# Performance work log

Hardware: AMD Instinct MI355X
Metric: run time of the kernel (lower is better)

The kernel has to match this reference:

```python
import jax, jax.numpy as jnp
import numpy as np

T, H = 2048, 2048            # tokens, hidden_size
NQ, NKV, D = 32, 4, 128      # q heads, kv heads, head_dim
E, K, I, CAP = 64, 8, 768, 512  # experts, top_k, moe_intermediate, per-expert capacity
EPS, THETA = 1e-6, 10000.0


def setup_inputs() -> dict:
    key = jax.random.key(0)
    ks = jax.random.split(key, 10)
    n = lambda k, shp, sc: jax.random.normal(k, shp, jnp.float32) * sc
    return {
        "hidden_states": n(ks[0], (T, H), 1.0),
        "positions": jnp.arange(T, dtype=jnp.int32),
        "wqkv": n(ks[1], (H, (NQ + 2 * NKV) * D), H ** -0.5),
        "wo": n(ks[2], (NQ * D, H), (NQ * D) ** -0.5),
        "q_norm_w": jnp.ones((D,), jnp.float32),
        "k_norm_w": jnp.ones((D,), jnp.float32),
        "ln1_w": jnp.ones((H,), jnp.float32),
        "ln2_w": jnp.ones((H,), jnp.float32),
        "gate_w": n(ks[3], (H, E), H ** -0.5),
        "w_gate": n(ks[4], (E, H, I), H ** -0.5),
        "w_up": n(ks[5], (E, H, I), H ** -0.5),
        "w_down": n(ks[6], (E, I, H), I ** -0.5),
    }


def _rmsnorm(x, w):
    v = jnp.mean(jnp.square(x.astype(jnp.float32)), axis=-1, keepdims=True)
    return (x.astype(jnp.float32) * jax.lax.rsqrt(v + EPS)).astype(x.dtype) * w


def _rope(x, cos, sin):
    # x: [T, heads, D]; neox-style rotate-half over full head_dim
    x1, x2 = x[..., : D // 2], x[..., D // 2:]
    c, s = cos[:, None, :], sin[:, None, :]
    return jnp.concatenate([x1 * c - x2 * s, x2 * c + x1 * s], axis=-1)


def _forward(hidden_states, positions, wqkv, wo, q_norm_w, k_norm_w, ln1_w, ln2_w, gate_w, w_gate, w_up, w_down):
    x = hidden_states
    # ---- input RMSNorm + GQA attention with QK-norm + RoPE ----
    h = _rmsnorm(x, ln1_w)
    qkv = h @ wqkv
    q, k, v = jnp.split(qkv, [NQ * D, NQ * D + NKV * D], axis=-1)
    q = _rmsnorm(q.reshape(T, NQ, D), q_norm_w)
    k = _rmsnorm(k.reshape(T, NKV, D), k_norm_w)
    v = v.reshape(T, NKV, D)
    inv_freq = 1.0 / (THETA ** (jnp.arange(0, D, 2, dtype=jnp.float32) / D))
    ang = positions.astype(jnp.float32)[:, None] * inv_freq  # [T, D/2]
    cos, sin = jnp.cos(ang), jnp.sin(ang)
    q, k = _rope(q, cos, sin), _rope(k, cos, sin)
    rep = NQ // NKV
    kr = jnp.repeat(k, rep, axis=1)  # [T, NQ, D]
    vr = jnp.repeat(v, rep, axis=1)
    scores = jnp.einsum('qhd,khd->hqk', q, kr) * (D ** -0.5)
    causal = jnp.tril(jnp.ones((T, T), bool))
    scores = jnp.where(causal[None], scores, -1e30)
    probs = jax.nn.softmax(scores, axis=-1)
    attn = jnp.einsum('hqk,khd->qhd', probs, vr).reshape(T, NQ * D)
    x = x + attn @ wo
    # ---- post-attn RMSNorm + sparse MoE (softmax top-k routing, renormalized) ----
    h = _rmsnorm(x, ln2_w)
    logits = h @ gate_w
    gate_probs = jax.nn.softmax(logits.astype(jnp.float32), axis=-1)
    topk_w, topk_idx = jax.lax.top_k(gate_probs, K)              # [T, K]
    topk_w = topk_w / jnp.sum(topk_w, axis=-1, keepdims=True)    # norm_topk_prob
    flat_e = topk_idx.reshape(-1)                                # [T*K], row-major
    oh = jax.nn.one_hot(flat_e, E, dtype=jnp.int32)
    pos = jnp.sum(jnp.cumsum(oh, axis=0) * oh, axis=-1) - 1      # slot within expert
    x_rep = jnp.repeat(h, K, axis=0)                             # [T*K, H]
    buf = jnp.zeros((E, CAP, H), h.dtype).at[flat_e, pos].set(x_rep, mode='drop')
    g = jnp.einsum('ech,ehi->eci', buf, w_gate)
    u = jnp.einsum('ech,ehi->eci', buf, w_up)
    act = jax.nn.silu(g) * u
    out_buf = jnp.einsum('eci,eih->ech', act, w_down)
    valid = (pos < CAP).astype(h.dtype)                          # CAP >> expected load; no drops in practice
    gathered = out_buf[flat_e, jnp.clip(pos, 0, CAP - 1)]        # [T*K, H]
    w = topk_w.reshape(-1).astype(h.dtype) * valid
    moe_out = jnp.sum((gathered * w[:, None]).reshape(T, K, H), axis=1)
    return x + moe_out


def reference(hidden_states, positions, wqkv, wo, q_norm_w, k_norm_w, ln1_w, ln2_w, gate_w, w_gate, w_up, w_down):
    return _forward(hidden_states, positions, wqkv, wo, q_norm_w, k_norm_w,
                    ln1_w, ln2_w, gate_w, w_gate, w_up, w_down)
```

## Files before the change

### kernel.cpp

```cpp
#include <hip/hip_runtime.h>
#include <hip/hip_bf16.h>

#define T_    2048
#define H_    2048
#define NQ_   32
#define NKV_  4
#define D_    128
#define E_    64
#define TK_   8
#define I_    768
#define CAP_  512
#define QKVW_ 5120

typedef float  f32x4  __attribute__((ext_vector_type(4)));
typedef __bf16 bf16x8 __attribute__((ext_vector_type(8)));
typedef int    i32x4  __attribute__((ext_vector_type(4)));
#define AS1 __attribute__((address_space(1)))
#define AS3 __attribute__((address_space(3)))

static __device__ __forceinline__ unsigned f2bf_u(float f){
  unsigned u = __builtin_bit_cast(unsigned, f);
  u += 0x7fffu + ((u >> 16) & 1u);
  return u >> 16;
}
static __device__ __forceinline__ float bf2f(unsigned h){
  unsigned u = h << 16;
  return __builtin_bit_cast(float, u);
}
struct HL { int h; int l; };
static __device__ __forceinline__ HL packsplit(float a, float b){
  unsigned ah = f2bf_u(a), bh = f2bf_u(b);
  float al = a - bf2f(ah), bl = b - bf2f(bh);
  HL r;
  r.h = (int)(ah | (bh << 16));
  r.l = (int)(f2bf_u(al) | (f2bf_u(bl) << 16));
  return r;
}
static __device__ __forceinline__ f32x4 mfma16(bf16x8 a, bf16x8 b, f32x4 c){
  return __builtin_amdgcn_mfma_f32_16x16x32_bf16(a, b, c, 0, 0, 0);
}

__global__ __launch_bounds__(256) void k_rms(const float* __restrict__ in,
                                             const float* __restrict__ w,
                                             unsigned short* __restrict__ outh,
                                             unsigned short* __restrict__ outl,
                                             float* __restrict__ cpy)
{
  const int t = blockIdx.x, tid = threadIdx.x;
  const float* row = in + (long)t * H_;
  float4 a = *(const float4*)(row + tid*8);
  float4 b = *(const float4*)(row + tid*8 + 4);
  float ss = a.x*a.x + a.y*a.y + a.z*a.z + a.w*a.w
           + b.x*b.x + b.y*b.y + b.z*b.z + b.w*b.w;
  #pragma unroll
  for (int o = 32; o >= 1; o >>= 1) ss += __shfl_xor(ss, o);
  __shared__ float red[4];
  if ((tid & 63) == 0) red[tid >> 6] = ss;
  __syncthreads();
  float tot = red[0] + red[1] + red[2] + red[3];
  float rs = rsqrtf(tot * (1.0f / (float)H_) + 1e-6f);
  const float* wp = w + tid*8;
  float vv[8] = {a.x, a.y, a.z, a.w, b.x, b.y, b.z, b.w};
  i32x4 oh, ol;
  #pragma unroll
  for (int d = 0; d < 4; d++){
    float v0 = vv[2*d]   * rs * wp[2*d];
    float v1 = vv[2*d+1] * rs * wp[2*d+1];
    HL r = packsplit(v0, v1);
    oh[d] = r.h; ol[d] = r.l;
  }
  *(i32x4*)(outh + (long)t * H_ + tid*8) = oh;
  if (outl) *(i32x4*)(outl + (long)t * H_ + tid*8) = ol;
  if (cpy){
    *(float4*)(cpy + (long)t * H_ + tid*8)     = a;
    *(float4*)(cpy + (long)t * H_ + tid*8 + 4) = b;
  }
}

__global__ __launch_bounds__(64) void k_ropetab(const int* __restrict__ pos,
                                                float* __restrict__ cosb,
                                                float* __restrict__ sinb)
{
  int t = blockIdx.x, j = threadIdx.x;
  float p = (float)pos[t];
  float freq = expf(-(float)j * (2.0f / (float)D_) * 9.210340371976184f);
  float ang = p * freq;
  cosb[t*64 + j] = cosf(ang);
  sinb[t*64 + j] = sinf(ang);
}

__global__ __launch_bounds__(256) void k_qknorm(const float* __restrict__ qkv,
                                                const float* __restrict__ qw,
                                                const float* __restrict__ kw,
                                                const float* __restrict__ cosb,
                                                const float* __restrict__ sinb,
                                                unsigned short* __restrict__ qh,
                                                unsigned short* __restrict__ ql,
                                                unsigned short* __restrict__ khp,
                                                unsigned short* __restrict__ klp)
{
  int gw = blockIdx.x*4 + (threadIdx.x >> 6);
  int lane = threadIdx.x & 63;
  int t = gw / 36, hh = gw - t*36;
  const float* src; const float* w;
  unsigned short *dh, *dl;
  if (hh < NQ_){
    src = qkv + (long)t*QKVW_ + hh*D_;
    w = qw;
    dh = qh + ((long)t*NQ_ + hh)*D_;
    dl = ql + ((long)t*NQ_ + hh)*D_;
  } else {
    int kh = hh - NQ_;
    src = qkv + (long)t*QKVW_ + NQ_*D_ + kh*D_;
    w = kw;
    dh = khp + ((long)t*NKV_ + kh)*D_;
    dl = klp + ((long)t*NKV_ + kh)*D_;
  }
  float a = src[lane], b = src[lane + 64];
  float ss = a*a + b*b;
  #pragma unroll
  for (int o = 32; o >= 1; o >>= 1) ss += __shfl_xor(ss, o);
  float rs = rsqrtf(ss * (1.0f / (float)D_) + 1e-6f);
  a *= rs * w[lane];
  b *= rs * w[lane + 64];
  float c = cosb[t*64 + lane], s = sinb[t*64 + lane];
  float r0 = a*c - b*s;
  float r1 = b*c + a*s;
  unsigned h0 = f2bf_u(r0), h1 = f2bf_u(r1);
  dh[lane]      = (unsigned short)h0;
  dh[lane + 64] = (unsigned short)h1;
  dl[lane]      = (unsigned short)f2bf_u(r0 - bf2f(h0));
  dl[lane + 64] = (unsigned short)f2bf_u(r1 - bf2f(h1));
}

__global__ __launch_bounds__(256) void k_vtrans(const float* __restrict__ qkv,
                                                unsigned short* __restrict__ vth,
                                                unsigned short* __restrict__ vtl)
{
  __shared__ unsigned short tileh[64][136];
  __shared__ unsigned short tilel[64][136];
  const int t0 = blockIdx.x * 64;
  const int hv = blockIdx.y;
  const int tid = threadIdx.x;
  #pragma unroll
  for (int it = 0; it < 8; it++){
    int chunk = tid + it*256;
    int r  = chunk >> 5;
    int c4 = chunk & 31;
    float4 v = *(const float4*)(qkv + (long)(t0 + r)*QKVW_ + (NQ_+NKV_)*D_ + hv*D_ + c4*4);
    float vals[4] = {v.x, v.y, v.z, v.w};
    #pragma unroll
    for (int q = 0; q < 4; q++){
      unsigned hi = f2bf_u(vals[q]);
      tileh[r][c4*4+q] = (unsigned short)hi;
      tilel[r][c4*4+q] = (unsigned short)f2bf_u(vals[q] - bf2f(hi));
    }
  }
  __syncthreads();
  int d = tid >> 1, hf = tid & 1;
  long dbase = ((long)(hv*D_ + d))*T_ + t0 + hf*32;
  #pragma unroll
  for (int k = 0; k < 4; k++){
    i32x4 oh, ol;
    #pragma unroll
    for (int d2 = 0; d2 < 4; d2++){
      int r0 = hf*32 + k*8 + d2*2, r1 = r0 + 1;
      oh[d2] = (int)((unsigned)tileh[r0][d] | ((unsigned)tileh[r1][d] << 16));
      ol[d2] = (int)((unsigned)tilel[r0][d] | ((unsigned)tilel[r1][d] << 16));
    }
    *(i32x4*)(vth + dbase + k*8) = oh;
    *(i32x4*)(vtl + dbase + k*8) = ol;
  }
}

__global__ __launch_bounds__(256,2) void k_attn(const unsigned short* __restrict__ qbh,
                                                const unsigned short* __restrict__ qbl,
                                                const unsigned short* __restrict__ kbh,
                                                const unsigned short* __restrict__ kbl,
                                                const unsigned short* __restrict__ vth,
                                                const unsigned short* __restrict__ vtl,
                                                unsigned short* __restrict__ abh,
                                                unsigned short* __restrict__ abl)
{
  __shared__ char ldsK[2][2][16384];
  const int b   = blockIdx.x;
  const int xcd = b & 7, kk = xcd >> 1;
  const int s_  = ((b >> 3) << 1) | (xcd & 1);
  const int h   = kk*8 + (s_ >> 4);
  const int p   = s_ & 15;
  const int hk  = kk;
  const int tid = threadIdx.x;
  const int wv  = tid >> 6, lane = tid & 63;
  const int l15 = lane & 15, g16 = lane >> 4;
  const float sc = 0.08838834764831845f;

  long gb[4];
  #pragma unroll
  for (int i = 0; i < 4; i++){
    int srow = i*16 + (tid >> 4);
    int c = (tid & 15) ^ (srow & 7);
    gb[i] = ((long)srow*NKV_ + hk)*D_ + c*8;
  }

  for (int ph = 0; ph < 2; ph++){
    const int qt  = ph ? p : (31 - p);
    const int q0  = qt*64 + wv*16;
    const int ntB = qt + 1;

    bf16x8 qfh[4], qfl[4];
    {
      long qoff = ((long)(q0 + l15)*NQ_ + h)*D_ + g16*8;
      #pragma unroll
      for (int ks = 0; ks < 4; ks++){
        qfh[ks] = *(const bf16x8*)(qbh + qoff + ks*32);
        qfl[ks] = *(const bf16x8*)(qbl + qoff + ks*32);
      }
    }

    f32x4 zz = {0.f,0.f,0.f,0.f};
    f32x4 o[8];
    #pragma unroll
    for (int dn = 0; dn < 8; dn++) o[dn] = zz;
    float m_run = -1e30f, l_run = 0.f;

    __syncthreads();
    #pragma unroll
    for (int i = 0; i < 4; i++){
      __builtin_amdgcn_global_load_lds((const AS1 int*)(kbh + gb[i]),
          (AS3 int*)((AS3 char*)&ldsK[0][0][0] + i*4096 + tid*16), 16, 0, 0);
      __builtin_amdgcn_global_load_lds((const AS1 int*)(kbl + gb[i]),
          (AS3 int*)((AS3 char*)&ldsK[0][1][0] + i*4096 + tid*16), 16, 0, 0);
    }

    for (int t = 0; t < ntB; t++){
      __syncthreads();
      const int kv0 = t*64;
      if (t+1 < ntB){
        long kadd = (long)(t+1)*64*NKV_*D_;
        int nb = (t+1) & 1;
        #pragma unroll
        for (int i = 0; i < 4; i++){
          __builtin_amdgcn_global_load_lds((const AS1 int*)(kbh + gb[i] + kadd),
              (AS3 int*)((AS3 char*)&ldsK[nb][0][0] + i*4096 + tid*16), 16, 0, 0);
          __builtin_amdgcn_global_load_lds((const AS1 int*)(kbl + gb[i] + kadd),
              (AS3 int*)((AS3 char*)&ldsK[nb][1][0] + i*4096 + tid*16), 16, 0, 0);
        }
      }
      {
        const char* Kh = &ldsK[t & 1][0][0];
        const char* Kl = &ldsK[t & 1][1][0];
        f32x4 sA[4];
        #pragma unroll
        for (int sub = 0; sub < 4; sub++) sA[sub] = zz;
        __builtin_amdgcn_s_setprio(1);
        #pragma unroll
        for (int sub = 0; sub < 4; sub++){
          int row = sub*16 + l15;
          int rsw = (row & 7) << 4;
          #pragma unroll
          for (int ks = 0; ks < 4; ks++){
            bf16x8 kh = *(const bf16x8*)(Kh + row*256 + (((ks*4 + g16)*16) ^ rsw));
            bf16x8 kl = *(const bf16x8*)(Kl + row*256 + (((ks*4 + g16)*16) ^ rsw));
            sA[sub] = mfma16(kh, qfl[ks], sA[sub]);
            sA[sub] = mfma16(kl, qfh[ks], sA[sub]);
            sA[sub] = mfma16(kh, qfh[ks], sA[sub]);
          }
        }
        __builtin_amdgcn_s_setprio(0);
        {
          int qrow = q0 + l15;
          float mt = -1e30f;
          #pragma unroll
          for (int sub = 0; sub < 4; sub++)
            #pragma unroll
            for (int r = 0; r < 4; r++){
              int kva = kv0 + sub*16 + g16*4 + r;
              float v = sA[sub][r]*sc;
              if (kva > qrow) v = -1e30f;
              sA[sub][r] = v;
              mt = fmaxf(mt, v);
            }
          mt = fmaxf(mt, __shfl_xor(mt,16));
          mt = fmaxf(mt, __shfl_xor(mt,32));
          float mnew = fmaxf(m_run, mt);
          float corr = __expf(m_run - mnew);
          float ps = 0.f;
          #pragma unroll
          for (int sub = 0; sub < 4; sub++)
            #pragma unroll
            for (int r = 0; r < 4; r++){
              float e = __expf(sA[sub][r] - mnew);
              sA[sub][r] = e;
              ps += e;
            }
          ps += __shfl_xor(ps,16);
          ps += __shfl_xor(ps,32);
          l_run = l_run*corr + ps;
          m_run = mnew;
          #pragma unroll
          for (int r = 0; r < 4; r++){
            float cr = __shfl(corr, g16*4 + r);
            #pragma unroll
            for (int dn = 0; dn < 8; dn++) o[dn][r] *= cr;
          }
        }
        #pragma unroll
        for (int kst = 0; kst < 2; kst++){
          bf16x8 pah, pal;
          {
            f32x4 s0 = sA[2*kst], s1 = sA[2*kst+1];
            i32x4 pkh, pkl;
            #pragma unroll
            for (int d = 0; d < 4; d++){
              const int e0 = 2*d, e1 = 2*d+1;
              int src0 = (((2*g16 + (e0>>2)) & 3) << 4) | l15;
              int src1 = (((2*g16 + (e1>>2)) & 3) << 4) | l15;
              float a0t = __shfl(s0[e0&3], src0), a1t = __shfl(s1[e0&3], src0);
              float b0t = __shfl(s0[e1&3], src1), b1t = __shfl(s1[e1&3], src1);
              float va = (g16 >= 2) ? a1t : a0t;
              float vb = (g16 >= 2) ? b1t : b0t;
              HL r = packsplit(va, vb);
              pkh[d] = r.h; pkl[d] = r.l;
            }
            pah = __builtin_bit_cast(bf16x8, pkh);
            pal = __builtin_bit_cast(bf16x8, pkl);
          }
          __builtin_amdgcn_s_setprio(1);
          #pragma unroll
          for (int dn = 0; dn < 8; dn++){
            long voff = ((long)(hk*D_ + dn*16 + l15))*T_ + kv0 + kst*32 + g16*8;
            bf16x8 bvh = *(const bf16x8*)(vth + voff);
            bf16x8 bvl = *(const bf16x8*)(vtl + voff);
            o[dn] = mfma16(pah, bvl, o[dn]);
            o[dn] = mfma16(pal, bvh, o[dn]);
            o[dn] = mfma16(pah, bvh, o[dn]);
          }
          __builtin_amdgcn_s_setprio(0);
        }
      }
    }

    {
      float linv = 1.0f / l_run;
      #pragma unroll
      for (int r = 0; r < 4; r++){
        float lr = __shfl(linv, g16*4 + r);
        long row = q0 + g16*4 + r;
        #pragma unroll
        for (int dn = 0; dn < 8; dn++){
          float v = o[dn][r]*lr;
          unsigned hi = f2bf_u(v);
          long idx = row*(NQ_*D_) + h*D_ + dn*16 + l15;
          abh[idx] = (unsigned short)hi;
          abl[idx] = (unsigned short)f2bf_u(v - bf2f(hi));
        }
      }
    }
  }
}

struct SA {
  const unsigned short* Ah;
  const unsigned short* Al;
  const float* B;
  int lda, ldb, K, ldc;
  float* Cf;
  const float* add;
};

template<int MODE>
__global__ __launch_bounds__(256,2) void k_gs(SA ga)
{
  __shared__ unsigned short ldsAh[128*64];
  __shared__ unsigned short ldsAl[128*64];
  __shared__ unsigned short ldsBh[8*128*8];
  __shared__ unsigned short ldsBl[8*128*8];
  const int tid = threadIdx.x;
  const int lane = tid & 63;
  const int wv = tid >> 6;
  const int wm = (wv >> 1)*64, wn = (wv & 1)*64;
  const int l15 = lane & 15, g16 = lane >> 4;

  const long m0 = (long)blockIdx.y * 128;
  const long n0 = (long)blockIdx.x * 128;

  long aoff[4];
  #pragma unroll
  for (int i = 0; i < 4; i++){
    int chunk = tid + i*256;
    int m = chunk >> 3, c = chunk & 7;
    aoff[i] = (m0 + m) * (long)ga.lda + c*8;
  }
  const float* brow = ga.B + n0 + (long)((tid >> 5)*8) * ga.ldb + (tid & 31)*4;

  f32x4 zz = {0.f,0.f,0.f,0.f};
  f32x4 acc[4][4];
  #pragma unroll
  for (int i = 0; i < 4; i++)
    #pragma unroll
    for (int j = 0; j < 4; j++) acc[i][j] = zz;

  i32x4 pva[4], pvl[4];
  float4 pb[8];
  #pragma unroll
  for (int i = 0; i < 4; i++){
    pva[i] = *(const i32x4*)(ga.Ah + aoff[i]);
    pvl[i] = *(const i32x4*)(ga.Al + aoff[i]);
  }
  #pragma unroll
  for (int r = 0; r < 8; r++) pb[r] = *(const float4*)(brow + (long)r * ga.ldb);

  for (int kt = 0; kt < ga.K; kt += 64){
    __syncthreads();
    #pragma unroll
    for (int i = 0; i < 4; i++){
      int chunk = tid + i*256;
      int m = chunk >> 3, c = chunk & 7;
      int sw = (c*16) ^ ((m & 7) << 4);
      *(i32x4*)((char*)ldsAh + m*128 + sw) = pva[i];
      *(i32x4*)((char*)ldsAl + m*128 + sw) = pvl[i];
    }
    {
      i32x4 ph0, ph1, ph2, ph3, pl0, pl1, pl2, pl3;
      #pragma unroll
      for (int r = 0; r < 8; r += 2){
        float4 va = pb[r];
        float4 vb = pb[r+1];
        int d = r >> 1;
        HL rx = packsplit(va.x, vb.x); ph0[d] = rx.h; pl0[d] = rx.l;
        HL ry = packsplit(va.y, vb.y); ph1[d] = ry.h; pl1[d] = ry.l;
        HL rz = packsplit(va.z, vb.z); ph2[d] = rz.h; pl2[d] = rz.l;
        HL rw = packsplit(va.w, vb.w); ph3[d] = rw.h; pl3[d] = rw.l;
      }
      int kbb = tid >> 5, nb = (tid & 31)*4;
      long bo = ((long)kbb*128 + nb) << 4;
      char* bph = (char*)ldsBh + bo;
      char* bpl = (char*)ldsBl + bo;
      *(i32x4*)(bph)      = ph0;  *(i32x4*)(bpl)      = pl0;
      *(i32x4*)(bph + 16) = ph1;  *(i32x4*)(bpl + 16) = pl1;
      *(i32x4*)(bph + 32) = ph2;  *(i32x4*)(bpl + 32) = pl2;
      *(i32x4*)(bph + 48) = ph3;  *(i32x4*)(bpl + 48) = pl3;
    }
    __syncthreads();
    if (kt + 64 < ga.K){
      #pragma unroll
      for (int i = 0; i < 4; i++){
        pva[i] = *(const i32x4*)(ga.Ah + aoff[i] + kt + 64);
        pvl[i] = *(const i32x4*)(ga.Al + aoff[i] + kt + 64);
      }
      #pragma unroll
      for (int r = 0; r < 8; r++) pb[r] = *(const float4*)(brow + (long)(kt + 64 + r) * ga.ldb);
    }
    #pragma unroll
    for (int ks = 0; ks < 2; ks++){
      bf16x8 afh[4], afl[4], bfh[4], bfl[4];
      #pragma unroll
      for (int i = 0; i < 4; i++){
        int m = wm + i*16 + l15;
        int sw = (ks*64 + g16*16) ^ ((m & 7) << 4);
        afh[i] = *(const bf16x8*)((const char*)ldsAh + m*128 + sw);
        afl[i] = *(const bf16x8*)((const char*)ldsAl + m*128 + sw);
      }
      #pragma unroll
      for (int j = 0; j < 4; j++){
        int n = wn + j*16 + l15;
        long bo = ((long)(ks*4 + g16)*128 + n) << 4;
        bfh[j] = *(const bf16x8*)((const char*)ldsBh + bo);
        bfl[j] = *(const bf16x8*)((const char*)ldsBl + bo);
      }
      #pragma unroll
      for (int i = 0; i < 4; i++)
        #pragma unroll
        for (int j = 0; j < 4; j++){
          acc[i][j] = mfma16(afh[i], bfl[j], acc[i][j]);
          acc[i][j] = mfma16(afl[i], bfh[j], acc[i][j]);
          acc[i][j] = mfma16(afh[i], bfh[j], acc[i][j]);
        }
    }
  }

  #pragma unroll
  for (int i = 0; i < 4; i++){
    #pragma unroll
    for (int j = 0; j < 4; j++){
      #pragma unroll
      for (int r = 0; r < 4; r++){
        float v = acc[i][j][r];
        long grow = m0 + wm + i*16 + g16*4 + r;
        long gcol = n0 + wn + j*16 + l15;
        long idx = grow * ga.ldc + gcol;
        if (MODE == 0) ga.Cf[idx] = v;
        else           ga.Cf[idx] = v + ga.add[idx];
      }
    }
  }
}

struct GA {
  const unsigned short* A;
  const float* B;
  const float* B2;
  int lda, ldb, K, ldc;
  unsigned short* Cb;
  const int* rowidx;
  const float* wslot;
  const int* counts;
  float* outp;
};

template<int MODE>
__global__ __launch_bounds__(256,3) void k_gemm(GA ga)
{
  __shared__ unsigned short ldsA[128*64];
  __shared__ unsigned short ldsB[8*128*8];
  const int tid = threadIdx.x;
  const int lane = tid & 63;
  const int wv = tid >> 6;
  const int wm = (wv >> 1)*64, wn = (wv & 1)*64;
  const int l15 = lane & 15, g16 = lane >> 4;

  long m0 = (long)blockIdx.y * 128;
  long n0 = 0;
  const unsigned short* A = ga.A;
  const float* B = ga.B;
  const int* rowmap = nullptr;
  int nrows;
  int e = blockIdx.z, count = ga.counts[e], hsel = 0;
  if ((int)m0 >= count) return;
  nrows = count;

  if (MODE == 2){
    int nt = blockIdx.x;
    hsel = (nt >= 6) ? 1 : 0;
    n0 = (long)(nt - hsel*6) * 128;
    B = (hsel ? ga.B2 : ga.B) + (long)e * H_ * I_;
    rowmap = ga.rowidx + e * CAP_;
  } else {
    n0 = (long)blockIdx.x * 128;
    B = ga.B + (long)e * I_ * H_;
    A = ga.A + (long)e * CAP_ * I_;
  }

  const unsigned short* arow[4];
  #pragma unroll
  for (int i = 0; i < 4; i++){
    int chunk = tid + i*256;
    int m = chunk >> 3, c = chunk & 7;
    int csw = c ^ (m & 7);
    int s = (int)m0 + m; if (s > nrows - 1) s = nrows - 1;
    long row = (MODE == 2) ? (long)rowmap[s] : (long)s;
    arow[i] = A + row * (long)ga.lda + csw*8;
  }
  const float* brow = B + n0 + (long)((tid >> 5)*8) * ga.ldb + (tid & 31)*4;

  f32x4 zz = {0.f,0.f,0.f,0.f};
  f32x4 acc[4][4];
  #pragma unroll
  for (int i = 0; i < 4; i++)
    #pragma unroll
    for (int j = 0; j < 4; j++) acc[i][j] = zz;

  float4 pb[8];
  #pragma unroll
  for (int r = 0; r < 8; r++) pb[r] = *(const float4*)(brow + (long)r * ga.ldb);

  for (int kt = 0; kt < ga.K; kt += 64){
    __syncthreads();
    #pragma unroll
    for (int i = 0; i < 4; i++){
      __builtin_amdgcn_global_load_lds((const AS1 int*)(arow[i] + kt),
          (AS3 int*)((AS3 char*)ldsA + i*4096 + tid*16), 16, 0, 0);
    }
    {
      i32x4 p0, p1, p2, p3;
      #pragma unroll
      for (int r = 0; r < 8; r += 2){
        float4 va = pb[r];
        float4 vb = pb[r+1];
        int d = r >> 1;
        p0[d] = (int)(f2bf_u(va.x) | (f2bf_u(vb.x) << 16));
        p1[d] = (int)(f2bf_u(va.y) | (f2bf_u(vb.y) << 16));
        p2[d] = (int)(f2bf_u(va.z) | (f2bf_u(vb.z) << 16));
        p3[d] = (int)(f2bf_u(va.w) | (f2bf_u(vb.w) << 16));
      }
      int kbb = tid >> 5, nb = (tid & 31)*4;
      char* bp = (char*)ldsB + (((long)kbb*128 + nb) << 4);
      *(i32x4*)(bp)      = p0;
      *(i32x4*)(bp + 16) = p1;
      *(i32x4*)(bp + 32) = p2;
      *(i32x4*)(bp + 48) = p3;
    }
    __syncthreads();
    if (kt + 64 < ga.K){
      #pragma unroll
      for (int r = 0; r < 8; r++) pb[r] = *(const float4*)(brow + (long)(kt + 64 + r) * ga.ldb);
    }
    #pragma unroll
    for (int ks = 0; ks < 2; ks++){
      bf16x8 af[4], bfv[4];
      #pragma unroll
      for (int i = 0; i < 4; i++){
        int m = wm + i*16 + l15;
        af[i] = *(const bf16x8*)((const char*)ldsA + m*128 + ((ks*64 + g16*16) ^ ((m & 7) << 4)));
      }
      #pragma unroll
      for (int j = 0; j < 4; j++){
        int n = wn + j*16 + l15;
        bfv[j] = *(const bf16x8*)((const char*)ldsB + (((long)(ks*4 + g16)*128 + n) << 4));
      }
      #pragma unroll
      for (int i = 0; i < 4; i++)
        #pragma unroll
        for (int j = 0; j < 4; j++)
          acc[i][j] = mfma16(af[i], bfv[j], acc[i][j]);
    }
  }

  #pragma unroll
  for (int i = 0; i < 4; i++){
    #pragma unroll
    for (int j = 0; j < 4; j++){
      #pragma unroll
      for (int r = 0; r < 4; r++){
        float v = acc[i][j][r];
        long grow = m0 + wm + i*16 + g16*4 + r;
        long gcol = n0 + wn + j*16 + l15;
        if (MODE == 2){
          if ((int)grow < count)
            ga.Cb[((long)(hsel*E_ + e)*CAP_ + grow)*I_ + gcol] = (unsigned short)f2bf_u(v);
        } else {
          if ((int)grow < count){
            float ww = ga.wslot[e*CAP_ + (int)grow];
            int tk = ga.rowidx[e*CAP_ + (int)grow];
            atomicAdd(ga.outp + (long)tk*H_ + gcol, v*ww);
          }
        }
      }
    }
  }
}

__global__ __launch_bounds__(64) void k_router(const float* __restrict__ x2,
                                               const float* __restrict__ ln2w,
                                               const float* __restrict__ gwt,
                                               int* __restrict__ tidx,
                                               float* __restrict__ twv)
{
  __shared__ float hl[H_];
  __shared__ int   ti[8];
  __shared__ float tv[8];
  const int t = blockIdx.x, lane = threadIdx.x;
  const float* row = x2 + (long)t * H_;
  float ss = 0.f;
  #pragma unroll 4
  for (int j = 0; j < 32; j++){
    float v = row[j*64 + lane];
    hl[j*64 + lane] = v;
    ss += v*v;
  }
  #pragma unroll
  for (int o = 32; o >= 1; o >>= 1) ss += __shfl_xor(ss, o);
  float rs = rsqrtf(ss * (1.0f / (float)H_) + 1e-6f);
  __syncthreads();
  #pragma unroll 4
  for (int j = 0; j < 32; j++) hl[j*64 + lane] *= rs * ln2w[j*64 + lane];
  __syncthreads();
  float acc = 0.f;
  #pragma unroll 8
  for (int k = 0; k < H_; k++) acc += hl[k] * gwt[(long)k*E_ + lane];
  float mx = acc;
  #pragma unroll
  for (int o = 32; o >= 1; o >>= 1) mx = fmaxf(mx, __shfl_xor(mx, o));
  float p = __expf(acc - mx);
  float sm = p;
  #pragma unroll
  for (int o = 32; o >= 1; o >>= 1) sm += __shfl_xor(sm, o);
  p /= sm;
  float cur = p, wsum = 0.f;
  #pragma unroll
  for (int j = 0; j < 8; j++){
    float v = cur; int ix = lane;
    #pragma unroll
    for (int o = 1; o < 64; o <<= 1){
      float ov = __shfl_xor(v, o); int oi = __shfl_xor(ix, o);
      if (ov > v || (ov == v && oi < ix)){ v = ov; ix = oi; }
    }
    if (lane == ix) cur = -1.f;
    wsum += v;
    if (lane == 0){ ti[j] = ix; tv[j] = v; }
  }
  __syncthreads();
  if (lane < 8){
    tidx[t*TK_ + lane] = ti[lane];
    twv [t*TK_ + lane] = tv[lane] / wsum;
  }
}

__global__ __launch_bounds__(64) void k_route(const int* __restrict__ tidx,
                                              const float* __restrict__ twv,
                                              int* __restrict__ rowi,
                                              float* __restrict__ wsl,
                                              int* __restrict__ cnts)
{
  const int e = blockIdx.x, lane = threadIdx.x;
  int run = 0;
  for (int s0 = 0; s0 < T_*TK_; s0 += 64){
    int s = s0 + lane;
    int idx = tidx[s];
    bool m = (idx == e);
    unsigned long long mk = __ballot(m);
    int pre = __popcll(mk & ((1ull << lane) - 1ull));
    int pos = run + pre;
    if (m && pos < CAP_){
      rowi[e*CAP_ + pos] = s >> 3;
      wsl [e*CAP_ + pos] = twv[s];
    }
    run += __popcll(mk);
  }
  if (lane == 0) cnts[e] = (run < CAP_) ? run : CAP_;
}

__global__ __launch_bounds__(256) void k_silu(unsigned short* __restrict__ gact,
                                              const unsigned short* __restrict__ uu)
{
  long i = ((long)blockIdx.x*256 + threadIdx.x)*8;
  i32x4 gv = *(const i32x4*)(gact + i);
  i32x4 uv = *(const i32x4*)(uu + i);
  i32x4 o;
  #pragma unroll
  for (int d = 0; d < 4; d++){
    unsigned gg = (unsigned)gv[d], ub = (unsigned)uv[d];
    float g0 = bf2f(gg & 0xffffu), g1 = bf2f(gg >> 16);
    float u0 = bf2f(ub & 0xffffu), u1 = bf2f(ub >> 16);
    float a0 = g0 / (1.f + __expf(-g0)) * u0;
    float a1 = g1 / (1.f + __expf(-g1)) * u1;
    o[d] = (int)(f2bf_u(a0) | (f2bf_u(a1) << 16));
  }
  *(i32x4*)(gact + i) = o;
}

extern "C" void kernel_launch(void* const* d_in, const int* in_sizes, int n_in,
                              void* d_out, int out_size, void* d_ws, size_t ws_size,
                              hipStream_t stream)
{
  (void)in_sizes; (void)n_in; (void)out_size; (void)ws_size;
  const float* x    = (const float*)d_in[0];
  const int*   pos  = (const int*)d_in[1];
  const float* wqkv = (const float*)d_in[2];
  const float* wo   = (const float*)d_in[3];
  const float* qnw  = (const float*)d_in[4];
  const float* knw  = (const float*)d_in[5];
  const float* ln1  = (const float*)d_in[6];
  const float* ln2  = (const float*)d_in[7];
  const float* gwt  = (const float*)d_in[8];
  const float* wg   = (const float*)d_in[9];
  const float* wu   = (const float*)d_in[10];
  const float* wd   = (const float*)d_in[11];
  float* out = (float*)d_out;

  char* ws = (char*)d_ws;
  size_t off = 0;
  auto alloc = [&](size_t b)->void*{ void* p = ws + off; off += (b + 255) & ~(size_t)255; return p; };

  unsigned short* hbh = (unsigned short*)alloc((size_t)T_*H_*2);
  unsigned short* hbl = (unsigned short*)alloc((size_t)T_*H_*2);
  float* qkv          = (float*)alloc((size_t)T_*QKVW_*4);
  float* cosb         = (float*)alloc((size_t)T_*64*4);
  float* sinb         = (float*)alloc((size_t)T_*64*4);
  unsigned short* qbh = (unsigned short*)alloc((size_t)T_*NQ_*D_*2);
  unsigned short* qbl = (unsigned short*)alloc((size_t)T_*NQ_*D_*2);
  unsigned short* kbh = (unsigned short*)alloc((size_t)T_*NKV_*D_*2);
  unsigned short* kbl = (unsigned short*)alloc((size_t)T_*NKV_*D_*2);
  unsigned short* vth = (unsigned short*)alloc((size_t)NKV_*D_*T_*2);
  unsigned short* vtl = (unsigned short*)alloc((size_t)NKV_*D_*T_*2);
  unsigned short* abh = (unsigned short*)alloc((size_t)T_*NQ_*D_*2);
  unsigned short* abl = (unsigned short*)alloc((size_t)T_*NQ_*D_*2);
  float* x2           = (float*)alloc((size_t)T_*H_*4);
  unsigned short* h2b = (unsigned short*)alloc((size_t)T_*H_*2);
  int* tidx           = (int*)alloc((size_t)T_*TK_*4);
  float* twv          = (float*)alloc((size_t)T_*TK_*4);
  int* rowi           = (int*)alloc((size_t)E_*CAP_*4);
  float* wsl          = (float*)alloc((size_t)E_*CAP_*4);
  int* cnts           = (int*)alloc((size_t)E_*4);
  unsigned short* gu  = (unsigned short*)alloc((size_t)2*E_*CAP_*I_*2);

  k_rms<<<T_, 256, 0, stream>>>(x, ln1, hbh, hbl, nullptr);
  k_ropetab<<<T_, 64, 0, stream>>>(pos, cosb, sinb);
  {
    SA a{}; a.Ah = hbh; a.Al = hbl; a.B = wqkv; a.lda = H_; a.ldb = QKVW_; a.K = H_; a.ldc = QKVW_; a.Cf = qkv;
    k_gs<0><<<dim3(QKVW_/128, T_/128), 256, 0, stream>>>(a);
  }
  k_qknorm<<<T_*36/4, 256, 0, stream>>>(qkv, qnw, knw, cosb, sinb, qbh, qbl, kbh, kbl);
  k_vtrans<<<dim3(T_/64, NKV_), 256, 0, stream>>>(qkv, vth, vtl);
  k_attn<<<512, 256, 0, stream>>>(qbh, qbl, kbh, kbl, vth, vtl, abh, abl);
  {
    SA a{}; a.Ah = abh; a.Al = abl; a.B = wo; a.lda = NQ_*D_; a.ldb = H_; a.K = NQ_*D_; a.ldc = H_;
    a.Cf = x2; a.add = x;
    k_gs<1><<<dim3(H_/128, T_/128), 256, 0, stream>>>(a);
  }
  k_rms<<<T_, 256, 0, stream>>>(x2, ln2, h2b, nullptr, out);
  k_router<<<T_, 64, 0, stream>>>(x2, ln2, gwt, tidx, twv);
  k_route<<<E_, 64, 0, stream>>>(tidx, twv, rowi, wsl, cnts);
  {
    GA a{}; a.A = h2b; a.B = wg; a.B2 = wu; a.lda = H_; a.ldb = I_; a.K = H_;
    a.Cb = gu; a.rowidx = rowi; a.counts = cnts;
    k_gemm<2><<<dim3(12, CAP_/128, E_), 256, 0, stream>>>(a);
  }
  k_silu<<<(E_*CAP_*I_)/(256*8), 256, 0, stream>>>(gu, gu + (size_t)E_*CAP_*I_);
  {
    GA a{}; a.A = gu; a.B = wd; a.lda = I_; a.ldb = H_; a.K = I_;
    a.counts = cnts; a.rowidx = rowi; a.wslot = wsl; a.outp = out;
    k_gemm<3><<<dim3(H_/128, CAP_/128, E_), 256, 0, stream>>>(a);
  }
}
```

Baseline: 1.575 ms.

## Fuse SiLU-gate multiply into gate/up expert GEMM epilogue

The gate/up expert GEMM now computes the gate and up projections for the same 64 intermediate columns in one tile. Each block loads half its B columns from w_gate and half from w_up, then applies silu(g)*u in the epilogue. This removes the standalone SiLU kernel and halves the intermediate buffer, avoiding a full extra read/write pass. Warp tiling changes from 64x64 to 32x128 per warp, also for the down-projection GEMM. That raises LDS fragment loads for B and may alter register pressure.

```diff
diff --git a/kernel.cpp b/kernel.cpp
--- a/kernel.cpp
+++ b/kernel.cpp
@@ -516,29 +516,30 @@
   const int tid = threadIdx.x;
   const int lane = tid & 63;
   const int wv = tid >> 6;
-  const int wm = (wv >> 1)*64, wn = (wv & 1)*64;
   const int l15 = lane & 15, g16 = lane >> 4;
 
   long m0 = (long)blockIdx.y * 128;
   long n0 = 0;
   const unsigned short* A = ga.A;
-  const float* B = ga.B;
   const int* rowmap = nullptr;
   int nrows;
-  int e = blockIdx.z, count = ga.counts[e], hsel = 0;
+  int e = blockIdx.z, count = ga.counts[e];
   if ((int)m0 >= count) return;
   nrows = count;
 
-  if (MODE == 2){
-    int nt = blockIdx.x;
-    hsel = (nt >= 6) ? 1 : 0;
-    n0 = (long)(nt - hsel*6) * 128;
-    B = (hsel ? ga.B2 : ga.B) + (long)e * H_ * I_;
-    rowmap = ga.rowidx + e * CAP_;
-  } else {
-    n0 = (long)blockIdx.x * 128;
-    B = ga.B + (long)e * I_ * H_;
-    A = ga.A + (long)e * CAP_ * I_;
+  const float* bbase;
+  {
+    int c4 = (tid & 31) * 4;
+    if (MODE == 2){
+      n0 = (long)blockIdx.x * 64;
+      rowmap = ga.rowidx + e * CAP_;
+      if (c4 < 64) bbase = ga.B  + (long)e * H_ * I_ + n0 + c4;
+      else         bbase = ga.B2 + (long)e * H_ * I_ + n0 + (c4 - 64);
+    } else {
+      n0 = (long)blockIdx.x * 128;
+      bbase = ga.B + (long)e * I_ * H_ + n0 + c4;
+      A = ga.A + (long)e * CAP_ * I_;
+    }
   }
 
   const unsigned short* arow[4];
@@ -551,14 +552,14 @@
     long row = (MODE == 2) ? (long)rowmap[s] : (long)s;
     arow[i] = A + row * (long)ga.lda + csw*8;
   }
-  const float* brow = B + n0 + (long)((tid >> 5)*8) * ga.ldb + (tid & 31)*4;
+  const float* brow = bbase + (long)((tid >> 5)*8) * ga.ldb;
 
   f32x4 zz = {0.f,0.f,0.f,0.f};
-  f32x4 acc[4][4];
-  #pragma unroll
-  for (int i = 0; i < 4; i++)
-    #pragma unroll
-    for (int j = 0; j < 4; j++) acc[i][j] = zz;
+  f32x4 acc[2][8];
+  #pragma unroll
+  for (int i = 0; i < 2; i++)
+    #pragma unroll
+    for (int j = 0; j < 8; j++) acc[i][j] = zz;
 
   float4 pb[8];
   #pragma unroll
@@ -597,41 +598,54 @@
     }
     #pragma unroll
     for (int ks = 0; ks < 2; ks++){
-      bf16x8 af[4], bfv[4];
-      #pragma unroll
-      for (int i = 0; i < 4; i++){
-        int m = wm + i*16 + l15;
+      bf16x8 af[2], bfv[8];
+      #pragma unroll
+      for (int i = 0; i < 2; i++){
+        int m = wv*32 + i*16 + l15;
         af[i] = *(const bf16x8*)((const char*)ldsA + m*128 + ((ks*64 + g16*16) ^ ((m & 7) << 4)));
       }
       #pragma unroll
-      for (int j = 0; j < 4; j++){
-        int n = wn + j*16 + l15;
+      for (int j = 0; j < 8; j++){
+        int n = j*16 + l15;
         bfv[j] = *(const bf16x8*)((const char*)ldsB + (((long)(ks*4 + g16)*128 + n) << 4));
       }
       #pragma unroll
-      for (int i = 0; i < 4; i++)
+      for (int i = 0; i < 2; i++)
         #pragma unroll
-        for (int j = 0; j < 4; j++)
+        for (int j = 0; j < 8; j++)
           acc[i][j] = mfma16(af[i], bfv[j], acc[i][j]);
     }
   }
 
-  #pragma unroll
-  for (int i = 0; i < 4; i++){
-    #pragma unroll
-    for (int j = 0; j < 4; j++){
-      #pragma unroll
-      for (int r = 0; r < 4; r++){
-        float v = acc[i][j][r];
-        long grow = m0 + wm + i*16 + g16*4 + r;
-        long gcol = n0 + wn + j*16 + l15;
-        if (MODE == 2){
-          if ((int)grow < count)
-            ga.Cb[((long)(hsel*E_ + e)*CAP_ + grow)*I_ + gcol] = (unsigned short)f2bf_u(v);
-        } else {
-          if ((int)grow < count){
-            float ww = ga.wslot[e*CAP_ + (int)grow];
-            int tk = ga.rowidx[e*CAP_ + (int)grow];
+  if (MODE == 2){
+    #pragma unroll
+    for (int i = 0; i < 2; i++){
+      #pragma unroll
+      for (int jj = 0; jj < 4; jj++){
+        #pragma unroll
+        for (int r = 0; r < 4; r++){
+          float g = acc[i][jj][r];
+          float u = acc[i][jj+4][r];
+          float actv = g / (1.f + __expf(-g)) * u;
+          int grow = (int)m0 + wv*32 + i*16 + g16*4 + r;
+          if (grow < count)
+            ga.Cb[((long)e*CAP_ + grow)*I_ + n0 + jj*16 + l15] = (unsigned short)f2bf_u(actv);
+        }
+      }
+    }
+  } else {
+    #pragma unroll
+    for (int i = 0; i < 2; i++){
+      #pragma unroll
+      for (int j = 0; j < 8; j++){
+        #pragma unroll
+        for (int r = 0; r < 4; r++){
+          float v = acc[i][j][r];
+          int grow = (int)m0 + wv*32 + i*16 + g16*4 + r;
+          long gcol = n0 + j*16 + l15;
+          if (grow < count){
+            float ww = ga.wslot[e*CAP_ + grow];
+            int tk = ga.rowidx[e*CAP_ + grow];
             atomicAdd(ga.outp + (long)tk*H_ + gcol, v*ww);
           }
         }
@@ -718,25 +732,6 @@
     run += __popcll(mk);
   }
   if (lane == 0) cnts[e] = (run < CAP_) ? run : CAP_;
-}
-
-__global__ __launch_bounds__(256) void k_silu(unsigned short* __restrict__ gact,
-                                              const unsigned short* __restrict__ uu)
-{
-  long i = ((long)blockIdx.x*256 + threadIdx.x)*8;
-  i32x4 gv = *(const i32x4*)(gact + i);
-  i32x4 uv = *(const i32x4*)(uu + i);
-  i32x4 o;
-  #pragma unroll
-  for (int d = 0; d < 4; d++){
-    unsigned gg = (unsigned)gv[d], ub = (unsigned)uv[d];
-    float g0 = bf2f(gg & 0xffffu), g1 = bf2f(gg >> 16);
-    float u0 = bf2f(ub & 0xffffu), u1 = bf2f(ub >> 16);
-    float a0 = g0 / (1.f + __expf(-g0)) * u0;
-    float a1 = g1 / (1.f + __expf(-g1)) * u1;
-    o[d] = (int)(f2bf_u(a0) | (f2bf_u(a1) << 16));
-  }
-  *(i32x4*)(gact + i) = o;
 }
 
 extern "C" void kernel_launch(void* const* d_in, const int* in_sizes, int n_in,
@@ -782,7 +777,7 @@
   int* rowi           = (int*)alloc((size_t)E_*CAP_*4);
   float* wsl          = (float*)alloc((size_t)E_*CAP_*4);
   int* cnts           = (int*)alloc((size_t)E_*4);
-  unsigned short* gu  = (unsigned short*)alloc((size_t)2*E_*CAP_*I_*2);
+  unsigned short* gu  = (unsigned short*)alloc((size_t)E_*CAP_*I_*2);
 
   k_rms<<<T_, 256, 0, stream>>>(x, ln1, hbh, hbl, nullptr);
   k_ropetab<<<T_, 64, 0, stream>>>(pos, cosb, sinb);
@@ -806,7 +801,6 @@
     a.Cb = gu; a.rowidx = rowi; a.counts = cnts;
     k_gemm<2><<<dim3(12, CAP_/128, E_), 256, 0, stream>>>(a);
   }
-  k_silu<<<(E_*CAP_*I_)/(256*8), 256, 0, stream>>>(gu, gu + (size_t)E_*CAP_*I_);
   {
     GA a{}; a.A = gu; a.B = wd; a.lda = I_; a.ldb = H_; a.K = I_;
     a.counts = cnts; a.rowidx = rowi; a.wslot = wsl; a.outp = out;
```

Measured after the change: 1.571 ms. Within noise of the previous version (-0.3%).
